# Kernel optimization log

Hardware: AMD Instinct MI355X
Metric: run time of the kernel (lower is better)

Reference implementation:

```python
import jax, jax.numpy as jnp
import numpy as np

B, S, D, H, F, L, V = 4, 512, 1024, 16, 4096, 6, 32000
HD = D // H
EPS = 1e-10


def layer_norm(x, g, b):
    m = x.mean(-1, keepdims=True)
    v = ((x - m) ** 2).mean(-1, keepdims=True)  # unbiased=False
    return g * (x - m) / jnp.sqrt(v + EPS) + b


def mha(q, k, v, wq, bq, wk, bk, wv, bv, wo, bo, mask):
    b_, s_, d_ = q.shape
    qh = (q @ wq + bq).reshape(b_, s_, H, HD).transpose(0, 2, 1, 3)  # [B,H,S,hd]
    kh = (k @ wk + bk).reshape(b_, s_, H, HD).transpose(0, 2, 1, 3)
    vh = (v @ wv + bv).reshape(b_, s_, H, HD).transpose(0, 2, 1, 3)
    score = jnp.einsum('bhqd,bhkd->bhqk', qh, kh) / jnp.sqrt(jnp.asarray(HD, q.dtype))
    score = jnp.where(mask == 0, jnp.asarray(-10000.0, q.dtype), score)
    attn = jax.nn.softmax(score, axis=-1)
    out = jnp.einsum('bhqk,bhkd->bhqd', attn, vh).transpose(0, 2, 1, 3).reshape(b_, s_, d_)
    return out @ wo + bo


def pos_encoding(seq, d):
    pos = jnp.arange(seq, dtype=jnp.float32)[:, None]
    i2 = jnp.arange(0, d, 2, dtype=jnp.float32)
    ang = pos / (10000.0 ** (i2 / d))
    enc = jnp.zeros((seq, d), jnp.float32)
    return enc.at[:, 0::2].set(jnp.sin(ang)).at[:, 1::2].set(jnp.cos(ang))


def setup_inputs() -> dict:
    key = jax.random.key(0)
    ks = iter(jax.random.split(key, 64))
    sd = 0.02
    inp = {
        'dec': jax.random.randint(next(ks), (B, S), 0, V),
        'enc': jax.random.normal(next(ks), (B, S, D), jnp.float32),
        't_mask': jnp.tril(jnp.ones((S, S), jnp.int32))[None, None],  # causal [1,1,S,S]
        's_mask': jnp.ones((1, 1, S, S), jnp.int32),
        'emb': (jax.random.normal(next(ks), (V, D), jnp.float32) * sd).at[1].set(0.0),  # padding_idx=1
    }
    for pre in ('sa', 'ca'):
        for nm in ('wq', 'wk', 'wv', 'wo'):
            inp[f'{pre}_{nm}'] = jax.random.normal(next(ks), (L, D, D), jnp.float32) * sd
            inp[f'{pre}_b{nm[1]}'] = jnp.zeros((L, D), jnp.float32)
    inp['ffn_w1'] = jax.random.normal(next(ks), (L, D, F), jnp.float32) * sd
    inp['ffn_b1'] = jnp.zeros((L, F), jnp.float32)
    inp['ffn_w2'] = jax.random.normal(next(ks), (L, F, D), jnp.float32) * sd
    inp['ffn_b2'] = jnp.zeros((L, D), jnp.float32)
    for i in (1, 2, 3):
        inp[f'ln{i}_g'] = jnp.ones((L, D), jnp.float32)
        inp[f'ln{i}_b'] = jnp.zeros((L, D), jnp.float32)
    inp['w_out'] = jax.random.normal(next(ks), (D, V), jnp.float32) * sd
    inp['b_out'] = jnp.zeros((V,), jnp.float32)
    return inp


def reference(dec, enc, t_mask, s_mask, emb,
              sa_wq, sa_bq, sa_wk, sa_bk, sa_wv, sa_bv, sa_wo, sa_bo,
              ca_wq, ca_bq, ca_wk, ca_bk, ca_wv, ca_bv, ca_wo, ca_bo,
              ffn_w1, ffn_b1, ffn_w2, ffn_b2,
              ln1_g, ln1_b, ln2_g, ln2_b, ln3_g, ln3_b, w_out, b_out):
    x = emb[dec] + pos_encoding(dec.shape[1], D)  # token + positional embedding
    for l in range(L):
        r = x
        a = mha(x, x, x, sa_wq[l], sa_bq[l], sa_wk[l], sa_bk[l], sa_wv[l], sa_bv[l], sa_wo[l], sa_bo[l], t_mask)
        x = layer_norm(a + r, ln1_g[l], ln1_b[l])
        r = x
        a = mha(x, enc, enc, ca_wq[l], ca_bq[l], ca_wk[l], ca_bk[l], ca_wv[l], ca_bv[l], ca_wo[l], ca_bo[l], s_mask)
        x = layer_norm(a + r, ln2_g[l], ln2_b[l])
        r = x
        f = jax.nn.relu(x @ ffn_w1[l] + ffn_b1[l]) @ ffn_w2[l] + ffn_b2[l]
        x = layer_norm(f + r, ln3_g[l], ln3_b[l])
    return x @ w_out + b_out  # [B,S,V] logits
```

## Files before the change

### kernel.cpp

```cpp
#include <hip/hip_runtime.h>
#include <hip/hip_bf16.h>
#include <math.h>

using bf16 = __hip_bfloat16;
typedef __attribute__((ext_vector_type(8))) short short8;
typedef __attribute__((ext_vector_type(4))) float f32x4;
typedef __attribute__((ext_vector_type(16))) float f32x16;

#define NTOKC 2048
#define DM 1024
#define SEQL 512
#define NHEADS 16
#define HDIM 64
#define FFDIM 4096
#define NLAYERS 6
#define VOCAB 32000

__device__ __forceinline__ void gld_lds16(const void* g, void* l) {
  __builtin_amdgcn_global_load_lds((__attribute__((address_space(1))) void*)g,
                                   (__attribute__((address_space(3))) void*)l, 16, 0, 0);
}

template<int BM, int BN>
__global__ __launch_bounds__(256, 3) void gemm_k(
    const bf16* __restrict__ A, const bf16* __restrict__ B, void* __restrict__ Cp,
    const float* __restrict__ bias, int K, int lda, int ldb, int ldc,
    long long sAb, long long sAh, long long sBb, long long sBh,
    long long sCb, long long sCh, int HH, int biasStride, float scale, int flags,
    int mTiles)
{
  constexpr int WAM = BM/64;
  constexpr int WAN = 4/WAM;
  constexpr int WN  = BN/WAN;
  constexpr int FM  = 2;
  constexpr int FN  = WN/32;
  constexpr int NCA = (BM*64)/2048;
  constexpr int NCB = (BN*64)/2048;
  __shared__ __align__(16) bf16 As[BM*64];
  __shared__ __align__(16) bf16 Bs[BN*64];
  const int tid = threadIdx.x, w = tid>>6, l = tid&63;
  const int z = blockIdx.z, zb = z/HH, zh = z - zb*HH;
  const bf16* Ab = A + (size_t)zb*sAb + (size_t)zh*sAh;
  const bf16* Bb = B + (size_t)zb*sBb + (size_t)zh*sBh;

  const int nwg = gridDim.x;
  int o = blockIdx.x, idx = o;
  if ((nwg & 7) == 0) idx = (o & 7) * (nwg >> 3) + (o >> 3);
  const int mt = idx % mTiles, nt = idx / mTiles;
  const int m0 = mt*BM, n0 = nt*BN;

  const int wm = w / WAN, wn = w % WAN;
  const int lr = l & 31;
  const int lh = l >> 5;

  f32x16 acc[FM][FN];
  #pragma unroll
  for (int i=0;i<FM;i++)
    #pragma unroll
    for (int j=0;j<FN;j++)
      #pragma unroll
      for (int e=0;e<16;e++) acc[i][j][e] = 0.f;

  int rA[NCA], kA[NCA];
  #pragma unroll
  for (int c=0;c<NCA;c++){ int e=c*2048+tid*8; int r=e>>6, k=e&63; rA[c]=r; kA[c]=k ^ ((r&7)<<3); }
  int rB[NCB], kB[NCB];
  #pragma unroll
  for (int c=0;c<NCB;c++){ int e=c*2048+tid*8; int r=e>>6, k=e&63; rB[c]=r; kB[c]=k ^ ((r&7)<<3); }

  for (int kt=0; kt<K; kt+=64) {
    #pragma unroll
    for (int c=0;c<NCA;c++)
      gld_lds16(Ab + (size_t)(m0+rA[c])*lda + kt + kA[c], (char*)As + c*4096 + w*1024);
    #pragma unroll
    for (int c=0;c<NCB;c++)
      gld_lds16(Bb + (size_t)(n0+rB[c])*ldb + kt + kB[c], (char*)Bs + c*4096 + w*1024);
    __syncthreads();
    #pragma unroll
    for (int kq=0; kq<4; kq++) {
      const int kk = kq*16 + lh*8;
      short8 a_[FM], b_[FN];
      #pragma unroll
      for (int i=0;i<FM;i++) {
        const int row = wm*64 + i*32 + lr;
        a_[i] = *(const short8*)(As + row*64 + (kk ^ ((row&7)<<3)));
      }
      #pragma unroll
      for (int j=0;j<FN;j++) {
        const int row = wn*WN + j*32 + lr;
        b_[j] = *(const short8*)(Bs + row*64 + (kk ^ ((row&7)<<3)));
      }
      #pragma unroll
      for (int i=0;i<FM;i++)
        #pragma unroll
        for (int j=0;j<FN;j++)
          acc[i][j] = __builtin_amdgcn_mfma_f32_32x32x16_bf16(a_[i], b_[j], acc[i][j], 0,0,0);
    }
    __syncthreads();
  }

  const bool obf = flags & 1, orl = flags & 2;
  const size_t coff = (size_t)zb*sCb + (size_t)zh*sCh;
  const float* brow = bias ? (bias + (size_t)z*biasStride) : nullptr;
  #pragma unroll
  for (int i=0;i<FM;i++) {
    #pragma unroll
    for (int j=0;j<FN;j++) {
      const int col = n0 + wn*WN + j*32 + lr;
      const float bv = brow ? brow[col] : 0.f;
      const int row0 = m0 + wm*64 + i*32 + 4*lh;
      #pragma unroll
      for (int r=0;r<16;r++) {
        const int row = row0 + (r&3) + 8*(r>>2);
        float v = acc[i][j][r]*scale + bv;
        if (orl) v = fmaxf(v, 0.f);
        const size_t off = coff + (size_t)row*ldc + col;
        if (obf) ((bf16*)Cp)[off] = __float2bfloat16(v);
        else     ((float*)Cp)[off] = v;
      }
    }
  }
}

template<int CAUSAL>
__global__ __launch_bounds__(256, 4) void flash_k(
    const bf16* __restrict__ Qg, const bf16* __restrict__ Kg,
    const bf16* __restrict__ Vt, bf16* __restrict__ Og)
{
  constexpr int PADK = 72;
  __shared__ __align__(16) bf16 Ks[64*PADK];
  __shared__ __align__(16) bf16 Vs[64*PADK];
  __shared__ __align__(16) bf16 Ps[4*16*PADK];
  const int tid = threadIdx.x, w = tid>>6, l = tid&63;
  const int qt = blockIdx.x, bh = blockIdx.y;
  const int b = bh>>4, h = bh&15;
  const int q0 = qt*64;
  const int lr = l&15, lg = l>>4;

  const bf16* qrow = Qg + (size_t)(b*SEQL + q0 + w*16 + lr)*DM + h*HDIM + lg*8;
  short8 qf0 = *(const short8*)(qrow);
  short8 qf1 = *(const short8*)(qrow + 32);

  const f32x4 vzero = {0.f,0.f,0.f,0.f};
  f32x4 Oa[4];
  float mrow[4], lrow[4];
  #pragma unroll
  for (int j=0;j<4;j++) Oa[j] = vzero;
  #pragma unroll
  for (int r=0;r<4;r++){ mrow[r] = -INFINITY; lrow[r] = 0.f; }

  const int ntiles = CAUSAL ? (qt+1) : (SEQL/64);
  const int c0 = tid, c1 = tid + 256;
  const int r0_ = c0>>3, o0_ = (c0&7)*8, r1_ = c1>>3, o1_ = (c1&7)*8;

  short8 s0,s1,s2,s3;
  {
    s0 = *(const short8*)(Kg + (size_t)(b*SEQL + r0_)*DM + h*HDIM + o0_);
    s1 = *(const short8*)(Kg + (size_t)(b*SEQL + r1_)*DM + h*HDIM + o1_);
    s2 = *(const short8*)(Vt + ((size_t)bh*HDIM + r0_)*SEQL + o0_);
    s3 = *(const short8*)(Vt + ((size_t)bh*HDIM + r1_)*SEQL + o1_);
  }

  for (int t=0; t<ntiles; ++t) {
    __syncthreads();
    *(short8*)(Ks + r0_*PADK + o0_) = s0;
    *(short8*)(Ks + r1_*PADK + o1_) = s1;
    *(short8*)(Vs + r0_*PADK + o0_) = s2;
    *(short8*)(Vs + r1_*PADK + o1_) = s3;
    __syncthreads();
    if (t+1 < ntiles) {
      const int kv1 = (t+1)*64;
      s0 = *(const short8*)(Kg + (size_t)(b*SEQL + kv1 + r0_)*DM + h*HDIM + o0_);
      s1 = *(const short8*)(Kg + (size_t)(b*SEQL + kv1 + r1_)*DM + h*HDIM + o1_);
      s2 = *(const short8*)(Vt + ((size_t)bh*HDIM + r0_)*SEQL + kv1 + o0_);
      s3 = *(const short8*)(Vt + ((size_t)bh*HDIM + r1_)*SEQL + kv1 + o1_);
    }

    f32x4 sa[4];
    #pragma unroll
    for (int jg=0;jg<4;jg++) {
      short8 kb0 = *(const short8*)(Ks + (jg*16+lr)*PADK + lg*8);
      short8 kb1 = *(const short8*)(Ks + (jg*16+lr)*PADK + 32 + lg*8);
      sa[jg] = __builtin_amdgcn_mfma_f32_16x16x32_bf16(qf0, kb0, vzero, 0,0,0);
      sa[jg] = __builtin_amdgcn_mfma_f32_16x16x32_bf16(qf1, kb1, sa[jg], 0,0,0);
    }

    float pv[4][4];
    #pragma unroll
    for (int jg=0;jg<4;jg++)
      #pragma unroll
      for (int r=0;r<4;r++) {
        float sv = sa[jg][r]*0.125f;
        if (CAUSAL && t==ntiles-1) {
          if (jg*16+lr > w*16+lg*4+r) sv = -INFINITY;
        }
        pv[jg][r] = sv;
      }
    float tm[4], sf[4], rs[4];
    #pragma unroll
    for (int r=0;r<4;r++) {
      float mx = fmaxf(fmaxf(pv[0][r],pv[1][r]), fmaxf(pv[2][r],pv[3][r]));
      #pragma unroll
      for (int o=1;o<16;o<<=1) mx = fmaxf(mx, __shfl_xor(mx, o));
      tm[r] = fmaxf(mrow[r], mx);
      sf[r] = __expf(mrow[r]-tm[r]);
      mrow[r] = tm[r];
    }
    #pragma unroll
    for (int r=0;r<4;r++) {
      float acc = 0.f;
      #pragma unroll
      for (int jg=0;jg<4;jg++) { float e = __expf(pv[jg][r]-tm[r]); pv[jg][r]=e; acc += e; }
      #pragma unroll
      for (int o=1;o<16;o<<=1) acc += __shfl_xor(acc, o);
      rs[r] = acc;
      lrow[r] = lrow[r]*sf[r] + rs[r];
    }
    #pragma unroll
    for (int jg=0;jg<4;jg++)
      #pragma unroll
      for (int r=0;r<4;r++) Oa[jg][r] *= sf[r];

    bf16* pw = Ps + w*16*PADK;
    #pragma unroll
    for (int jg=0;jg<4;jg++)
      #pragma unroll
      for (int r=0;r<4;r++)
        pw[(lg*4+r)*PADK + jg*16+lr] = __float2bfloat16(pv[jg][r]);
    asm volatile("s_waitcnt lgkmcnt(0)" ::: "memory");
    __builtin_amdgcn_sched_barrier(0);
    short8 pa0 = *(const short8*)(pw + lr*PADK + lg*8);
    short8 pa1 = *(const short8*)(pw + lr*PADK + 32 + lg*8);
    #pragma unroll
    for (int jg=0;jg<4;jg++) {
      short8 vb0 = *(const short8*)(Vs + (jg*16+lr)*PADK + lg*8);
      short8 vb1 = *(const short8*)(Vs + (jg*16+lr)*PADK + 32 + lg*8);
      Oa[jg] = __builtin_amdgcn_mfma_f32_16x16x32_bf16(pa0, vb0, Oa[jg], 0,0,0);
      Oa[jg] = __builtin_amdgcn_mfma_f32_16x16x32_bf16(pa1, vb1, Oa[jg], 0,0,0);
    }
  }

  #pragma unroll
  for (int r=0;r<4;r++) {
    const float inv = 1.f/lrow[r];
    const size_t rb = (size_t)(b*SEQL + q0 + w*16 + lg*4 + r)*DM + h*HDIM;
    #pragma unroll
    for (int jg=0;jg<4;jg++)
      Og[rb + jg*16 + lr] = __float2bfloat16(Oa[jg][r]*inv);
  }
}

__global__ __launch_bounds__(256) void embed_k(const int* __restrict__ dec, const float* __restrict__ emb,
    float* __restrict__ x32, bf16* __restrict__ x16)
{
  const int idx = blockIdx.x*256 + threadIdx.x;
  const int d = idx & (DM-1), tok = idx >> 10, s = tok & (SEQL-1);
  const float e = emb[(size_t)dec[tok]*DM + d];
  const float den = powf(10000.f, (float)(d & ~1) * (1.f/(float)DM));
  const float ang = (float)s / den;
  const float pe = (d&1) ? cosf(ang) : sinf(ang);
  const float vv = e + pe;
  x32[idx] = vv; x16[idx] = __float2bfloat16(vv);
}

__global__ __launch_bounds__(256) void cvt_k(const float* __restrict__ in, bf16* __restrict__ out, int n){
  int i = blockIdx.x*256 + threadIdx.x;
  if (i < n) out[i] = __float2bfloat16(in[i]);
}

__global__ __launch_bounds__(256) void trans_k(const float* __restrict__ src, bf16* __restrict__ dst, int K, int N)
{
  __shared__ float t[32][33];
  const int n0 = blockIdx.x*32, k0 = blockIdx.y*32;
  const int tx = threadIdx.x&31, ty = threadIdx.x>>5;
  #pragma unroll
  for (int i=0;i<4;i++) t[ty+i*8][tx] = src[(size_t)(k0+ty+i*8)*N + n0+tx];
  __syncthreads();
  #pragma unroll
  for (int i=0;i<4;i++) dst[(size_t)(n0+ty+i*8)*K + k0+tx] = __float2bfloat16(t[tx][ty+i*8]);
}

struct TPack { const float* src[10]; bf16* dst[10]; int K[10]; int N[10]; int tile0[10]; };
__global__ __launch_bounds__(256) void transm_k(TPack p)
{
  __shared__ float t[32][33];
  const int id = blockIdx.x;
  int mi = 0;
  #pragma unroll
  for (int i=1;i<10;i++) if (id >= p.tile0[i]) mi = i;
  const float* src = p.src[mi]; bf16* dst = p.dst[mi];
  const int K = p.K[mi], N = p.N[mi];
  const int local = id - p.tile0[mi];
  const int ntn = N >> 5;
  const int nt = local % ntn, kt = local / ntn;
  const int n0 = nt*32, k0 = kt*32;
  const int tx = threadIdx.x&31, ty = threadIdx.x>>5;
  #pragma unroll
  for (int i=0;i<4;i++) t[ty+i*8][tx] = src[(size_t)(k0+ty+i*8)*N + n0+tx];
  __syncthreads();
  #pragma unroll
  for (int i=0;i<4;i++) dst[(size_t)(n0+ty+i*8)*K + k0+tx] = __float2bfloat16(t[tx][ty+i*8]);
}

struct BiasSrc { const float* s[5]; float* out; };
__global__ __launch_bounds__(256) void biaspack_k(BiasSrc p)
{
  const int i = blockIdx.x*256 + threadIdx.x;
  const int l = i / 5120, j = i - l*5120;
  const int m = j >> 10, c = j & 1023;
  p.out[i] = p.s[m][(size_t)l*DM + c];
}

__global__ __launch_bounds__(256) void vtrans_k(const bf16* __restrict__ v, bf16* __restrict__ vt)
{
  __shared__ bf16 t[32][33];
  const int bh = blockIdx.z, b = bh>>4, h = bh&15;
  const int s0 = blockIdx.x*32, d0 = blockIdx.y*32;
  const int tx = threadIdx.x&31, ty = threadIdx.x>>5;
  #pragma unroll
  for (int i=0;i<4;i++)
    t[ty+i*8][tx] = v[(size_t)(b*SEQL + s0+ty+i*8)*DM + h*HDIM + d0+tx];
  __syncthreads();
  #pragma unroll
  for (int i=0;i<4;i++)
    vt[((size_t)bh*HDIM + d0+ty+i*8)*SEQL + s0+tx] = t[tx][ty+i*8];
}

__global__ __launch_bounds__(256) void ln_k(const float* __restrict__ a, const float* __restrict__ r,
    const float* __restrict__ g, const float* __restrict__ be,
    float* __restrict__ y32, bf16* __restrict__ y16)
{
  const int row = blockIdx.x, t = threadIdx.x;
  const size_t base = (size_t)row*DM;
  float v[4]; float s = 0.f;
  #pragma unroll
  for (int i=0;i<4;i++){ int c=t+i*256; v[i] = a[base+c] + r[base+c]; s += v[i]; }
  __shared__ float red[8];
  #pragma unroll
  for (int o=32;o>0;o>>=1) s += __shfl_down(s,o);
  if ((t&63)==0) red[t>>6]=s;
  __syncthreads();
  const float mean = (red[0]+red[1]+red[2]+red[3]) * (1.f/1024.f);
  float vs = 0.f;
  #pragma unroll
  for (int i=0;i<4;i++){ float d=v[i]-mean; vs += d*d; }
  #pragma unroll
  for (int o=32;o>0;o>>=1) vs += __shfl_down(vs,o);
  if ((t&63)==0) red[4+(t>>6)]=vs;
  __syncthreads();
  const float var = (red[4]+red[5]+red[6]+red[7]) * (1.f/1024.f);
  const float rstd = rsqrtf(var + 1e-10f);
  #pragma unroll
  for (int i=0;i<4;i++){
    int c=t+i*256;
    float y = g[c]*(v[i]-mean)*rstd + be[c];
    y32[base+c] = y; y16[base+c] = __float2bfloat16(y);
  }
}

template<int CAUSAL>
static void run_attention(hipStream_t st, bf16* qkv, bf16* vt, bf16* ctx)
{
  vtrans_k<<<dim3(16,2,64),256,0,st>>>(qkv + (size_t)2*NTOKC*DM, vt);
  flash_k<CAUSAL><<<dim3(SEQL/64, 64),256,0,st>>>(qkv, qkv + (size_t)NTOKC*DM, vt, ctx);
}

extern "C" void kernel_launch(void* const* d_in, const int* in_sizes, int n_in,
                              void* d_out, int out_size, void* d_ws, size_t ws_size,
                              hipStream_t stream)
{
  (void)in_sizes; (void)n_in; (void)out_size;
  const int*   dec    = (const int*)  d_in[0];
  const float* enc    = (const float*)d_in[1];
  const float* emb    = (const float*)d_in[4];
  const float* sa_w[4] = { (const float*)d_in[5], (const float*)d_in[7], (const float*)d_in[9],  (const float*)d_in[11] };
  const float* sa_b[4] = { (const float*)d_in[6], (const float*)d_in[8], (const float*)d_in[10], (const float*)d_in[12] };
  const float* ca_w[4] = { (const float*)d_in[13], (const float*)d_in[15], (const float*)d_in[17], (const float*)d_in[19] };
  const float* ca_b[4] = { (const float*)d_in[14], (const float*)d_in[16], (const float*)d_in[18], (const float*)d_in[20] };
  const float* ffn_w1 = (const float*)d_in[21];
  const float* ffn_b1 = (const float*)d_in[22];
  const float* ffn_w2 = (const float*)d_in[23];
  const float* ffn_b2 = (const float*)d_in[24];
  const float* ln_g[3] = { (const float*)d_in[25], (const float*)d_in[27], (const float*)d_in[29] };
  const float* ln_b[3] = { (const float*)d_in[26], (const float*)d_in[28], (const float*)d_in[30] };
  const float* w_out  = (const float*)d_in[31];
  const float* b_out  = (const float*)d_in[32];
  float* out = (float*)d_out;

  char* p = (char*)d_ws;
  auto alloc = [&](size_t b)->char* { char* r=p; p += (b+255)&~(size_t)255; return r; };
  bf16* x16   = (bf16*)alloc((size_t)NTOKC*DM*2);
  bf16* enc16 = (bf16*)alloc((size_t)NTOKC*DM*2);
  bf16* qkv   = (bf16*)alloc((size_t)3*NTOKC*DM*2);
  bf16* ctx   = (bf16*)alloc((size_t)NTOKC*DM*2);
  bf16* vt    = (bf16*)alloc((size_t)64*HDIM*SEQL*2);
  bf16* mid   = (bf16*)alloc((size_t)NTOKC*FFDIM*2);
  bf16* wtA   = (bf16*)alloc((size_t)8*DM*DM*2);
  bf16* wtF1  = (bf16*)alloc((size_t)FFDIM*DM*2);
  bf16* wtF2  = (bf16*)alloc((size_t)DM*FFDIM*2);
  bf16* wtO   = (bf16*)alloc((size_t)VOCAB*DM*2);
  float* x32  = (float*)alloc((size_t)NTOKC*DM*4);
  float* aout = (float*)alloc((size_t)NTOKC*DM*4);
  float* biasAll = (float*)alloc((size_t)NLAYERS*5*DM*4);
  if ((size_t)(p - (char*)d_ws) > ws_size) return;

  embed_k<<<8192,256,0,stream>>>(dec, emb, x32, x16);
  cvt_k<<<8192,256,0,stream>>>(enc, enc16, NTOKC*DM);
  trans_k<<<dim3(VOCAB/32, DM/32),256,0,stream>>>(w_out, wtO, DM, VOCAB);
  {
    BiasSrc bs;
    bs.s[0]=sa_b[0]; bs.s[1]=sa_b[1]; bs.s[2]=sa_b[2]; bs.s[3]=ca_b[1]; bs.s[4]=ca_b[2];
    bs.out = biasAll;
    biaspack_k<<<(NLAYERS*5*DM)/256,256,0,stream>>>(bs);
  }

  for (int l=0; l<NLAYERS; ++l) {
    {
      TPack tp;
      for (int i=0;i<4;i++){ tp.src[i]   = sa_w[i] + (size_t)l*DM*DM; tp.dst[i]   = wtA + (size_t)i*DM*DM;
                             tp.K[i]=DM; tp.N[i]=DM; tp.tile0[i]=i*1024; }
      for (int i=0;i<4;i++){ tp.src[4+i] = ca_w[i] + (size_t)l*DM*DM; tp.dst[4+i] = wtA + (size_t)(4+i)*DM*DM;
                             tp.K[4+i]=DM; tp.N[4+i]=DM; tp.tile0[4+i]=(4+i)*1024; }
      tp.src[8]=ffn_w1 + (size_t)l*DM*FFDIM; tp.dst[8]=wtF1; tp.K[8]=DM; tp.N[8]=FFDIM; tp.tile0[8]=8192;
      tp.src[9]=ffn_w2 + (size_t)l*FFDIM*DM; tp.dst[9]=wtF2; tp.K[9]=FFDIM; tp.N[9]=DM; tp.tile0[9]=12288;
      transm_k<<<16384,256,0,stream>>>(tp);
    }
    const float* biasL = biasAll + (size_t)l*5*DM;

    gemm_k<128,128><<<dim3(128,1,3),256,0,stream>>>(x16, wtA, qkv, biasL,
        DM, DM, DM, DM, 0,0, (long long)DM*DM,0, (long long)NTOKC*DM,0, 1, DM, 1.f, 1, 16);
    run_attention<1>(stream, qkv, vt, ctx);
    gemm_k<64,128><<<dim3(256,1,1),256,0,stream>>>(ctx, wtA + (size_t)3*DM*DM, aout, sa_b[3]+l*DM,
        DM, DM, DM, DM, 0,0,0,0,0,0, 1, 0, 1.f, 0, 32);
    ln_k<<<2048,256,0,stream>>>(aout, x32, ln_g[0]+l*DM, ln_b[0]+l*DM, x32, x16);

    gemm_k<64,128><<<dim3(256,1,1),256,0,stream>>>(x16, wtA + (size_t)4*DM*DM, qkv, ca_b[0]+l*DM,
        DM, DM, DM, DM, 0,0,0,0,0,0, 1, 0, 1.f, 1, 32);
    gemm_k<128,128><<<dim3(128,1,2),256,0,stream>>>(enc16, wtA + (size_t)5*DM*DM, qkv + (size_t)NTOKC*DM, biasL + 3*DM,
        DM, DM, DM, DM, 0,0, (long long)DM*DM,0, (long long)NTOKC*DM,0, 1, DM, 1.f, 1, 16);
    run_attention<0>(stream, qkv, vt, ctx);
    gemm_k<64,128><<<dim3(256,1,1),256,0,stream>>>(ctx, wtA + (size_t)7*DM*DM, aout, ca_b[3]+l*DM,
        DM, DM, DM, DM, 0,0,0,0,0,0, 1, 0, 1.f, 0, 32);
    ln_k<<<2048,256,0,stream>>>(aout, x32, ln_g[1]+l*DM, ln_b[1]+l*DM, x32, x16);

    gemm_k<128,128><<<dim3(512,1,1),256,0,stream>>>(x16, wtF1, mid, ffn_b1 + (size_t)l*FFDIM,
        DM, DM, DM, FFDIM, 0,0,0,0,0,0, 1, 0, 1.f, 1|2, 16);
    gemm_k<64,128><<<dim3(256,1,1),256,0,stream>>>(mid, wtF2, aout, ffn_b2 + (size_t)l*DM,
        FFDIM, FFDIM, FFDIM, DM, 0,0,0,0,0,0, 1, 0, 1.f, 0, 32);
    ln_k<<<2048,256,0,stream>>>(aout, x32, ln_g[2]+l*DM, ln_b[2]+l*DM, x32, x16);
  }

  gemm_k<128,128><<<dim3(4000,1,1),256,0,stream>>>(x16, wtO, out, b_out,
      DM, DM, DM, VOCAB, 0,0,0,0,0,0, 1, 0, 1.f, 0, 16);
}
```

Before: 1.845 ms.

## Double-buffer GEMM LDS tiles with 32-wide K stages and raise occupancy

```diff
diff --git a/kernel.cpp b/kernel.cpp
--- a/kernel.cpp
+++ b/kernel.cpp
@@ -22,7 +22,7 @@
 }
 
 template<int BM, int BN>
-__global__ __launch_bounds__(256, 3) void gemm_k(
+__global__ __launch_bounds__(256, 4) void gemm_k(
     const bf16* __restrict__ A, const bf16* __restrict__ B, void* __restrict__ Cp,
     const float* __restrict__ bias, int K, int lda, int ldb, int ldc,
     long long sAb, long long sAh, long long sBb, long long sBh,
@@ -34,10 +34,10 @@
   constexpr int WN  = BN/WAN;
   constexpr int FM  = 2;
   constexpr int FN  = WN/32;
-  constexpr int NCA = (BM*64)/2048;
-  constexpr int NCB = (BN*64)/2048;
-  __shared__ __align__(16) bf16 As[BM*64];
-  __shared__ __align__(16) bf16 Bs[BN*64];
+  constexpr int NCA = BM/64;
+  constexpr int NCB = BN/64;
+  __shared__ __align__(16) bf16 As[2*BM*32];
+  __shared__ __align__(16) bf16 Bs[2*BN*32];
   const int tid = threadIdx.x, w = tid>>6, l = tid&63;
   const int z = blockIdx.z, zb = z/HH, zh = z - zb*HH;
   const bf16* Ab = A + (size_t)zb*sAb + (size_t)zh*sAh;
@@ -63,32 +63,37 @@
 
   int rA[NCA], kA[NCA];
   #pragma unroll
-  for (int c=0;c<NCA;c++){ int e=c*2048+tid*8; int r=e>>6, k=e&63; rA[c]=r; kA[c]=k ^ ((r&7)<<3); }
+  for (int c=0;c<NCA;c++){ int e=c*2048+tid*8; int r=e>>5, k=e&31; rA[c]=r; kA[c]=k ^ ((r&3)<<3); }
   int rB[NCB], kB[NCB];
   #pragma unroll
-  for (int c=0;c<NCB;c++){ int e=c*2048+tid*8; int r=e>>6, k=e&63; rB[c]=r; kB[c]=k ^ ((r&7)<<3); }
-
-  for (int kt=0; kt<K; kt+=64) {
+  for (int c=0;c<NCB;c++){ int e=c*2048+tid*8; int r=e>>5, k=e&31; rB[c]=r; kB[c]=k ^ ((r&3)<<3); }
+
+  auto stage = [&](int buf, int kt) {
     #pragma unroll
     for (int c=0;c<NCA;c++)
-      gld_lds16(Ab + (size_t)(m0+rA[c])*lda + kt + kA[c], (char*)As + c*4096 + w*1024);
+      gld_lds16(Ab + (size_t)(m0+rA[c])*lda + kt + kA[c],
+                (char*)As + buf*(BM*64) + c*4096 + w*1024);
     #pragma unroll
     for (int c=0;c<NCB;c++)
-      gld_lds16(Bb + (size_t)(n0+rB[c])*ldb + kt + kB[c], (char*)Bs + c*4096 + w*1024);
-    __syncthreads();
-    #pragma unroll
-    for (int kq=0; kq<4; kq++) {
+      gld_lds16(Bb + (size_t)(n0+rB[c])*ldb + kt + kB[c],
+                (char*)Bs + buf*(BN*64) + c*4096 + w*1024);
+  };
+  auto compute = [&](int buf) {
+    const bf16* Ap = As + buf*(BM*32);
+    const bf16* Bp = Bs + buf*(BN*32);
+    #pragma unroll
+    for (int kq=0; kq<2; kq++) {
       const int kk = kq*16 + lh*8;
       short8 a_[FM], b_[FN];
       #pragma unroll
       for (int i=0;i<FM;i++) {
         const int row = wm*64 + i*32 + lr;
-        a_[i] = *(const short8*)(As + row*64 + (kk ^ ((row&7)<<3)));
+        a_[i] = *(const short8*)(Ap + row*32 + (kk ^ ((row&3)<<3)));
       }
       #pragma unroll
       for (int j=0;j<FN;j++) {
         const int row = wn*WN + j*32 + lr;
-        b_[j] = *(const short8*)(Bs + row*64 + (kk ^ ((row&7)<<3)));
+        b_[j] = *(const short8*)(Bp + row*32 + (kk ^ ((row&3)<<3)));
       }
       #pragma unroll
       for (int i=0;i<FM;i++)
@@ -96,7 +101,16 @@
         for (int j=0;j<FN;j++)
           acc[i][j] = __builtin_amdgcn_mfma_f32_32x32x16_bf16(a_[i], b_[j], acc[i][j], 0,0,0);
     }
+  };
+
+  stage(0, 0);
+  for (int kt = 0; kt < K; kt += 64) {
     __syncthreads();
+    stage(1, kt+32);
+    compute(0);
+    __syncthreads();
+    if (kt + 64 < K) stage(0, kt+64);
+    compute(1);
   }
 
   const bool obf = flags & 1, orl = flags & 2;
```

After: 2.055 ms. 1.11x slower.

## Add 256x256-tile 8-wave GEMM kernel for final vocab projection

Applied to the files above, without the earlier changes.

```diff
diff --git a/kernel.cpp b/kernel.cpp
--- a/kernel.cpp
+++ b/kernel.cpp
@@ -115,6 +115,109 @@
         float v = acc[i][j][r]*scale + bv;
         if (orl) v = fmaxf(v, 0.f);
         const size_t off = coff + (size_t)row*ldc + col;
+        if (obf) ((bf16*)Cp)[off] = __float2bfloat16(v);
+        else     ((float*)Cp)[off] = v;
+      }
+    }
+  }
+}
+
+__global__ __launch_bounds__(512, 2) void gemm8_k(
+    const bf16* __restrict__ A, const bf16* __restrict__ B, void* __restrict__ Cp,
+    const float* __restrict__ bias, int K, int lda, int ldb, int ldc,
+    float scale, int flags, int mTiles)
+{
+  extern __shared__ __align__(16) char smem[];
+  bf16* As = (bf16*)smem;
+  bf16* Bs = As + 2*256*64;
+  const int tid = threadIdx.x, w = tid>>6, l = tid&63;
+
+  const int nwg = gridDim.x;
+  int o = blockIdx.x, idx = o;
+  if ((nwg & 7) == 0) idx = (o & 7) * (nwg >> 3) + (o >> 3);
+  const int mt = idx % mTiles, nt = idx / mTiles;
+  const int m0 = mt*256, n0 = nt*256;
+
+  const int wm = w>>2, wn = w&3;
+  const int lr = l&31, lh = l>>5;
+
+  f32x16 acc[4][2];
+  #pragma unroll
+  for (int i=0;i<4;i++)
+    #pragma unroll
+    for (int j=0;j<2;j++)
+      #pragma unroll
+      for (int e=0;e<16;e++) acc[i][j][e] = 0.f;
+
+  int rr[4], kk_[4];
+  #pragma unroll
+  for (int c=0;c<4;c++){ int e=c*4096+tid*8; int r=e>>6, k=e&63; rr[c]=r; kk_[c]=k ^ ((r&7)<<3); }
+
+  auto stage = [&](int buf, int kt) {
+    #pragma unroll
+    for (int c=0;c<4;c++)
+      gld_lds16(A + (size_t)(m0+rr[c])*lda + kt + kk_[c],
+                (char*)As + buf*32768 + c*8192 + w*1024);
+    #pragma unroll
+    for (int c=0;c<4;c++)
+      gld_lds16(B + (size_t)(n0+rr[c])*ldb + kt + kk_[c],
+                (char*)Bs + buf*32768 + c*8192 + w*1024);
+  };
+
+  stage(0, 0);
+  const int ntk = K >> 6;
+  for (int t=0; t<ntk; ++t) {
+    const int buf = t & 1;
+    if (t+1 < ntk) {
+      stage(buf^1, (t+1)<<6);
+      asm volatile("s_waitcnt vmcnt(8)" ::: "memory");
+    } else {
+      asm volatile("s_waitcnt vmcnt(0)" ::: "memory");
+    }
+    __builtin_amdgcn_sched_barrier(0);
+    __builtin_amdgcn_s_barrier();
+    const bf16* Ap = As + buf*16384;
+    const bf16* Bp = Bs + buf*16384;
+    #pragma unroll
+    for (int kq=0; kq<4; kq++) {
+      const int kk = kq*16 + lh*8;
+      short8 a_[4], b_[2];
+      #pragma unroll
+      for (int i=0;i<4;i++) {
+        const int row = wm*128 + i*32 + lr;
+        a_[i] = *(const short8*)(Ap + row*64 + (kk ^ ((row&7)<<3)));
+      }
+      #pragma unroll
+      for (int j=0;j<2;j++) {
+        const int row = wn*64 + j*32 + lr;
+        b_[j] = *(const short8*)(Bp + row*64 + (kk ^ ((row&7)<<3)));
+      }
+      __builtin_amdgcn_s_setprio(1);
+      #pragma unroll
+      for (int i=0;i<4;i++)
+        #pragma unroll
+        for (int j=0;j<2;j++)
+          acc[i][j] = __builtin_amdgcn_mfma_f32_32x32x16_bf16(a_[i], b_[j], acc[i][j], 0,0,0);
+      __builtin_amdgcn_s_setprio(0);
+    }
+    __builtin_amdgcn_sched_barrier(0);
+    __builtin_amdgcn_s_barrier();
+  }
+
+  const bool obf = flags & 1, orl = flags & 2;
+  #pragma unroll
+  for (int i=0;i<4;i++) {
+    #pragma unroll
+    for (int j=0;j<2;j++) {
+      const int col = n0 + wn*64 + j*32 + lr;
+      const float bv = bias ? bias[col] : 0.f;
+      const int row0 = m0 + wm*128 + i*32 + 4*lh;
+      #pragma unroll
+      for (int r=0;r<16;r++) {
+        const int row = row0 + (r&3) + 8*(r>>2);
+        float v = acc[i][j][r]*scale + bv;
+        if (orl) v = fmaxf(v, 0.f);
+        const size_t off = (size_t)row*ldc + col;
         if (obf) ((bf16*)Cp)[off] = __float2bfloat16(v);
         else     ((float*)Cp)[off] = v;
       }
@@ -450,6 +553,6 @@
     ln_k<<<2048,256,0,stream>>>(aout, x32, ln_g[2]+l*DM, ln_b[2]+l*DM, x32, x16);
   }
 
-  gemm_k<128,128><<<dim3(4000,1,1),256,0,stream>>>(x16, wtO, out, b_out,
-      DM, DM, DM, VOCAB, 0,0,0,0,0,0, 1, 0, 1.f, 0, 16);
-}
+  gemm8_k<<<dim3(1000), 512, 131072, stream>>>(x16, wtO, out, b_out,
+      DM, DM, DM, VOCAB, 1.f, 0, 8);
+}
```

New measurement: 1.844 ms. Within noise of the previous version (-0.1%).
